# Kernel tuning notes

Hardware: AMD Instinct MI355X
Metric: run time of the kernel (lower is better)

Reference implementation:

```python
import jax, jax.numpy as jnp
import numpy as np

B_, C_, H_, W_ = 4, 96, 256, 256
COUT = 96  # c2


def dwt(x):
    # Haar decompose over 2x2 blocks; names mirror the torch code:
    # x1_1 = even-row/even-col, x2_1 = odd-row/even-col,
    # x1_2 = even-row/odd-col,  x2_2 = odd-row/odd-col (all /2).
    x1_1 = x[:, :, 0::2, 0::2] * 0.5
    x2_1 = x[:, :, 1::2, 0::2] * 0.5
    x1_2 = x[:, :, 0::2, 1::2] * 0.5
    x2_2 = x[:, :, 1::2, 1::2] * 0.5
    A = x1_1 + x2_1 + x1_2 + x2_2
    Bc = -x1_1 - x2_1 + x1_2 + x2_2
    Cc = -x1_1 + x2_1 - x1_2 + x2_2
    D = x1_1 - x2_1 - x1_2 + x2_2
    return A, Bc, Cc, D


def idwt(A, Bc, Cc, D):
    q = 0.25
    x1_1 = (A - Bc - Cc + D) * q
    x2_1 = (A - Bc + Cc - D) * q
    x1_2 = (A + Bc - Cc - D) * q
    x2_2 = (A + Bc + Cc + D) * q
    b, c, h, w = x1_1.shape
    # interleave columns: x1[:, :, :, 0::2]=x1_1, x1[:, :, :, 1::2]=x1_2
    x1 = jnp.stack([x1_1, x1_2], axis=-1).reshape(b, c, h, 2 * w)
    x2 = jnp.stack([x2_1, x2_2], axis=-1).reshape(b, c, h, 2 * w)
    # interleave rows with the *2 scaling from the torch code
    x = jnp.stack([x1 * 2.0, x2 * 2.0], axis=3).reshape(b, c, 2 * h, 2 * w)
    return x


def ffm(a, b):
    # mask*a + (1-mask)*b with binary mask == select
    return jnp.where(jnp.abs(a) >= jnp.abs(b), a, b)


def setup_inputs() -> dict:
    key = jax.random.key(0)
    k1, k2, k3, kw = jax.random.split(key, 4)
    shp = (B_, C_, H_, W_)
    x1 = jax.random.normal(k1, shp, dtype=jnp.float32)
    x2 = jax.random.normal(k2, shp, dtype=jnp.float32)
    x3 = jax.random.normal(k3, shp, dtype=jnp.float32)
    w_out = jax.random.normal(kw, (COUT, 3 * C_), dtype=jnp.float32) / np.sqrt(3 * C_).astype(np.float32)
    return {"x1": x1, "x2": x2, "x3": x3, "w_out": w_out}


def reference(x1, x2, x3, w_out):
    # same channels / same even HxW -> no align conv, no interpolate, no pad
    A1, B1, C1, D1 = dwt(x1)
    A2, B2, C2, D2 = dwt(x2)
    A3, B3, C3, D3 = dwt(x3)
    A = (A1 + A2 + A3) / 3.0
    Bb = ffm(ffm(B1, B2), B3)
    Cc = ffm(ffm(C1, C2), C3)
    Dd = ffm(ffm(D1, D2), D3)
    x_rec = idwt(A, Bb, Cc, Dd)
    y = jnp.concatenate([x_rec, x2, x3], axis=1)  # [B, 3C, H, W]
    return jnp.einsum('bchw,oc->bohw', y, w_out)  # 1x1 conv, no bias
```

## Files before the change

### kernel.cpp

```cpp
#include <hip/hip_runtime.h>

constexpr int NB = 4, NC = 96, NH = 256, NW = 256;
constexpr int NK = 288;
constexpr int HW = NH * NW;

typedef __attribute__((ext_vector_type(8))) short short8;
typedef __attribute__((ext_vector_type(4))) float f32x4;

__device__ __forceinline__ unsigned short f2bf(float f) {
    unsigned int u = __builtin_bit_cast(unsigned int, f);
    u += 0x7FFFu + ((u >> 16) & 1u);
    return (unsigned short)(u >> 16);
}

__device__ __forceinline__ float ffm_sel(float a, float b) {
    return (__builtin_fabsf(a) >= __builtin_fabsf(b)) ? a : b;
}

__global__ __launch_bounds__(256) void dwt_fused_kernel(
    const float* __restrict__ x1, const float* __restrict__ x2,
    const float* __restrict__ x3, const float* __restrict__ w_out,
    float* __restrict__ out)
{
    __shared__ __align__(16) unsigned short y_lds[3][64][40];
    __shared__ __align__(16) unsigned short w_lds[3][96][40];

    const int tid  = threadIdx.x;
    const int wv   = tid >> 6;
    const int lane = tid & 63;
    const int n    = lane & 15;
    const int q    = lane >> 4;
    const int bx = blockIdx.x, by = blockIdx.y, bz = blockIdx.z;

    f32x4 acc[6];
#pragma unroll
    for (int t = 0; t < 6; ++t) acc[t] = (f32x4){0.f, 0.f, 0.f, 0.f};

    const int cp = tid >> 4, cb = tid & 15;
    const int gx = bx * 32 + 2 * cb;
    const int h0 = by * 2;

    for (int s = 0; s < 3; ++s) {
        const int ch0 = 32 * s;

#pragma unroll
        for (int j = 0; j < 9; ++j) {
            int i = tid + (j << 8);
            int row = i >> 3, part = i & 7;
            int sec = (row >= 192) ? 2 : (row >= 96 ? 1 : 0);
            int o = row - sec * 96;
            float4 v = *(const float4*)(w_out + (size_t)o * NK + sec * 96 + ch0 + part * 4);
            *(ushort4*)&w_lds[sec][o][part * 4] =
                make_ushort4(f2bf(v.x), f2bf(v.y), f2bf(v.z), f2bf(v.w));
        }

        float xr[2][4], r2[2][4], r3[2][4];
#pragma unroll
        for (int dc = 0; dc < 2; ++dc) {
            const int c = ch0 + 2 * cp + dc;
            const size_t base = ((size_t)(bz * NC + c) * NH + h0) * NW + gx;
            float2 a1 = *(const float2*)(x1 + base);
            float2 b1 = *(const float2*)(x1 + base + NW);
            float2 a2 = *(const float2*)(x2 + base);
            float2 b2 = *(const float2*)(x2 + base + NW);
            float2 a3 = *(const float2*)(x3 + base);
            float2 b3 = *(const float2*)(x3 + base + NW);

            float A1, B1, C1, D1, A2, B2, C2, D2, A3, B3, C3, D3;
#define DWT4(aa, bb, Ao, Bo, Co, Do)                                          \
            { float e = aa.x * 0.5f, f = bb.x * 0.5f,                          \
                    g = aa.y * 0.5f, h = bb.y * 0.5f;                          \
              Ao = ((e + f) + g) + h;  Bo = (((-e) - f) + g) + h;              \
              Co = (((-e) + f) - g) + h; Do = ((e - f) - g) + h; }
            DWT4(a1, b1, A1, B1, C1, D1)
            DWT4(a2, b2, A2, B2, C2, D2)
            DWT4(a3, b3, A3, B3, C3, D3)
#undef DWT4
            float A  = (A1 + A2 + A3) / 3.0f;
            float Bf = ffm_sel(ffm_sel(B1, B2), B3);
            float Cf = ffm_sel(ffm_sel(C1, C2), C3);
            float Df = ffm_sel(ffm_sel(D1, D2), D3);
            xr[dc][0] = (((A - Bf) - Cf) + Df) * 0.5f;
            xr[dc][1] = (((A - Bf) + Cf) - Df) * 0.5f;
            xr[dc][2] = (((A + Bf) - Cf) - Df) * 0.5f;
            xr[dc][3] = (((A + Bf) + Cf) + Df) * 0.5f;
            r2[dc][0] = a2.x; r2[dc][1] = b2.x; r2[dc][2] = a2.y; r2[dc][3] = b2.y;
            r3[dc][0] = a3.x; r3[dc][1] = b3.x; r3[dc][2] = a3.y; r3[dc][3] = b3.y;
        }
        const int pxs[4] = {2 * cb, 32 + 2 * cb, 2 * cb + 1, 33 + 2 * cb};
#pragma unroll
        for (int p = 0; p < 4; ++p) {
            *(ushort2*)&y_lds[0][pxs[p]][2 * cp] = make_ushort2(f2bf(xr[0][p]), f2bf(xr[1][p]));
            *(ushort2*)&y_lds[1][pxs[p]][2 * cp] = make_ushort2(f2bf(r2[0][p]), f2bf(r2[1][p]));
            *(ushort2*)&y_lds[2][pxs[p]][2 * cp] = make_ushort2(f2bf(r3[0][p]), f2bf(r3[1][p]));
        }

        __syncthreads();

#pragma unroll
        for (int sec = 0; sec < 3; ++sec) {
            short8 bfrag = *(const short8*)&y_lds[sec][16 * wv + n][q * 8];
#pragma unroll
            for (int t = 0; t < 6; ++t) {
                short8 afrag = *(const short8*)&w_lds[sec][16 * t + n][q * 8];
                acc[t] = __builtin_amdgcn_mfma_f32_16x16x32_bf16(afrag, bfrag, acc[t], 0, 0, 0);
            }
        }

        __syncthreads();
    }

    const int row  = wv >> 1;
    const int colb = 16 * (wv & 1) + n;
    const int h    = 2 * by + row;
    const int wc   = 32 * bx + colb;
#pragma unroll
    for (int t = 0; t < 6; ++t) {
#pragma unroll
        for (int r = 0; r < 4; ++r) {
            int o = 16 * t + 4 * q + r;
            out[(size_t)(bz * NC + o) * HW + h * NW + wc] = acc[t][r];
        }
    }
}

extern "C" void kernel_launch(void* const* d_in, const int* in_sizes, int n_in,
                              void* d_out, int out_size, void* d_ws, size_t ws_size,
                              hipStream_t stream) {
    const float* x1 = (const float*)d_in[0];
    const float* x2 = (const float*)d_in[1];
    const float* x3 = (const float*)d_in[2];
    const float* w  = (const float*)d_in[3];
    float* out = (float*)d_out;
    dim3 grid(NW / 32, NH / 2, NB);
    dwt_fused_kernel<<<grid, dim3(256), 0, stream>>>(x1, x2, x3, w, out);
}
```

Measured before the change: 352.5 us.

## Keep weights in registers, loop over row-pairs with double-buffered swizzled LDS

Each block now processes 8 row-pairs with 384 threads instead of one row-pair with 256. The bf16 weight fragments are loaded once into registers per wave (each wave owns 16 output channels), so the per-block LDS weight staging and conversion go away. Global loads for the next row-pair are issued before the current MFMAs, and the staging uses a double-buffered, XOR-swizzled LDS tile that holds all 288 channels at once. The cost is higher register pressure (9 weight fragments plus 36 prefetch floats), a larger LDS footprint, and fewer blocks in the grid.

```diff
diff --git a/kernel.cpp b/kernel.cpp
--- a/kernel.cpp
+++ b/kernel.cpp
@@ -3,6 +3,8 @@
 constexpr int NB = 4, NC = 96, NH = 256, NW = 256;
 constexpr int NK = 288;
 constexpr int HW = NH * NW;
+constexpr int RPB = 8;
+constexpr int ROWB = 640;
 
 typedef __attribute__((ext_vector_type(8))) short short8;
 typedef __attribute__((ext_vector_type(4))) float f32x4;
@@ -17,109 +19,152 @@
     return (__builtin_fabsf(a) >= __builtin_fabsf(b)) ? a : b;
 }
 
-__global__ __launch_bounds__(256) void dwt_fused_kernel(
+__global__ __launch_bounds__(384, 3) void dwt_fused_kernel(
     const float* __restrict__ x1, const float* __restrict__ x2,
     const float* __restrict__ x3, const float* __restrict__ w_out,
     float* __restrict__ out)
 {
-    __shared__ __align__(16) unsigned short y_lds[3][64][40];
-    __shared__ __align__(16) unsigned short w_lds[3][96][40];
+    __shared__ __align__(16) unsigned char y_lds[2][64 * ROWB];
 
     const int tid  = threadIdx.x;
     const int wv   = tid >> 6;
     const int lane = tid & 63;
-    const int n    = lane & 15;
-    const int q    = lane >> 4;
+    const int n = lane & 15;
+    const int q = lane >> 4;
     const int bx = blockIdx.x, by = blockIdx.y, bz = blockIdx.z;
 
-    f32x4 acc[6];
+    short8 wfrag[9];
+    {
+        const float* wr = w_out + (size_t)(16 * wv + n) * NK + 8 * q;
 #pragma unroll
-    for (int t = 0; t < 6; ++t) acc[t] = (f32x4){0.f, 0.f, 0.f, 0.f};
+        for (int c9 = 0; c9 < 9; ++c9) {
+            float4 lo = *(const float4*)(wr + 32 * c9);
+            float4 hi = *(const float4*)(wr + 32 * c9 + 4);
+            short8 f;
+            f[0] = (short)f2bf(lo.x); f[1] = (short)f2bf(lo.y);
+            f[2] = (short)f2bf(lo.z); f[3] = (short)f2bf(lo.w);
+            f[4] = (short)f2bf(hi.x); f[5] = (short)f2bf(hi.y);
+            f[6] = (short)f2bf(hi.z); f[7] = (short)f2bf(hi.w);
+            wfrag[c9] = f;
+        }
+    }
 
-    const int cp = tid >> 4, cb = tid & 15;
-    const int gx = bx * 32 + 2 * cb;
-    const int h0 = by * 2;
+    const int cp = tid >> 3;
+    const int cq = tid & 7;
+    const int gx = bx * 32 + 4 * cq;
+    const float* xs[3] = {x1, x2, x3};
 
-    for (int s = 0; s < 3; ++s) {
-        const int ch0 = 32 * s;
+    float4 pf[3][2][2];
 
+    auto issue = [&](int rp) {
+        const int h0 = 2 * (by * RPB + rp);
 #pragma unroll
-        for (int j = 0; j < 9; ++j) {
-            int i = tid + (j << 8);
-            int row = i >> 3, part = i & 7;
-            int sec = (row >= 192) ? 2 : (row >= 96 ? 1 : 0);
-            int o = row - sec * 96;
-            float4 v = *(const float4*)(w_out + (size_t)o * NK + sec * 96 + ch0 + part * 4);
-            *(ushort4*)&w_lds[sec][o][part * 4] =
-                make_ushort4(f2bf(v.x), f2bf(v.y), f2bf(v.z), f2bf(v.w));
+        for (int a = 0; a < 3; ++a) {
+#pragma unroll
+            for (int dc = 0; dc < 2; ++dc) {
+                const int c = 2 * cp + dc;
+                const size_t base = ((size_t)(bz * NC + c) * NH + h0) * NW + gx;
+                pf[a][dc][0] = *(const float4*)(xs[a] + base);
+                pf[a][dc][1] = *(const float4*)(xs[a] + base + NW);
+            }
         }
+    };
 
-        float xr[2][4], r2[2][4], r3[2][4];
+    auto stage = [&](int buf) {
+        unsigned char* Y = y_lds[buf];
 #pragma unroll
-        for (int dc = 0; dc < 2; ++dc) {
-            const int c = ch0 + 2 * cp + dc;
-            const size_t base = ((size_t)(bz * NC + c) * NH + h0) * NW + gx;
-            float2 a1 = *(const float2*)(x1 + base);
-            float2 b1 = *(const float2*)(x1 + base + NW);
-            float2 a2 = *(const float2*)(x2 + base);
-            float2 b2 = *(const float2*)(x2 + base + NW);
-            float2 a3 = *(const float2*)(x3 + base);
-            float2 b3 = *(const float2*)(x3 + base + NW);
+        for (int hf = 0; hf < 2; ++hf) {
+            const int cb = 2 * cq + hf;
+            float xr[2][4], r2[2][4], r3[2][4];
+#pragma unroll
+            for (int dc = 0; dc < 2; ++dc) {
+                float2 a1, b1, a2, b2, a3, b3;
+                if (hf == 0) {
+                    a1 = make_float2(pf[0][dc][0].x, pf[0][dc][0].y);
+                    b1 = make_float2(pf[0][dc][1].x, pf[0][dc][1].y);
+                    a2 = make_float2(pf[1][dc][0].x, pf[1][dc][0].y);
+                    b2 = make_float2(pf[1][dc][1].x, pf[1][dc][1].y);
+                    a3 = make_float2(pf[2][dc][0].x, pf[2][dc][0].y);
+                    b3 = make_float2(pf[2][dc][1].x, pf[2][dc][1].y);
+                } else {
+                    a1 = make_float2(pf[0][dc][0].z, pf[0][dc][0].w);
+                    b1 = make_float2(pf[0][dc][1].z, pf[0][dc][1].w);
+                    a2 = make_float2(pf[1][dc][0].z, pf[1][dc][0].w);
+                    b2 = make_float2(pf[1][dc][1].z, pf[1][dc][1].w);
+                    a3 = make_float2(pf[2][dc][0].z, pf[2][dc][0].w);
+                    b3 = make_float2(pf[2][dc][1].z, pf[2][dc][1].w);
+                }
+                float A1, B1, C1, D1, A2, B2, C2, D2, A3, B3, C3, D3;
+#define DWT4(aa, bb, Ao, Bo, Co, Do)                                          \
+                { float e = aa.x * 0.5f, fE = bb.x * 0.5f,                     \
+                        g = aa.y * 0.5f, hE = bb.y * 0.5f;                     \
+                  Ao = ((e + fE) + g) + hE;  Bo = (((-e) - fE) + g) + hE;      \
+                  Co = (((-e) + fE) - g) + hE; Do = ((e - fE) - g) + hE; }
+                DWT4(a1, b1, A1, B1, C1, D1)
+                DWT4(a2, b2, A2, B2, C2, D2)
+                DWT4(a3, b3, A3, B3, C3, D3)
+#undef DWT4
+                float A  = (A1 + A2 + A3) / 3.0f;
+                float Bf = ffm_sel(ffm_sel(B1, B2), B3);
+                float Cf = ffm_sel(ffm_sel(C1, C2), C3);
+                float Df = ffm_sel(ffm_sel(D1, D2), D3);
+                xr[dc][0] = (((A - Bf) - Cf) + Df) * 0.5f;
+                xr[dc][1] = (((A - Bf) + Cf) - Df) * 0.5f;
+                xr[dc][2] = (((A + Bf) - Cf) - Df) * 0.5f;
+                xr[dc][3] = (((A + Bf) + Cf) + Df) * 0.5f;
+                r2[dc][0] = a2.x; r2[dc][1] = b2.x; r2[dc][2] = a2.y; r2[dc][3] = b2.y;
+                r3[dc][0] = a3.x; r3[dc][1] = b3.x; r3[dc][2] = a3.y; r3[dc][3] = b3.y;
+            }
+            const int pxs[4] = {2 * cb, 32 + 2 * cb, 2 * cb + 1, 33 + 2 * cb};
+#pragma unroll
+            for (int p = 0; p < 4; ++p) {
+                const int px = pxs[p];
+                unsigned char* rowp = Y + px * ROWB;
+                const int sw = ((px ^ (px >> 3)) & 7) << 4;
+                *(ushort2*)(rowp + ((      4 * cp) ^ sw)) = make_ushort2(f2bf(xr[0][p]), f2bf(xr[1][p]));
+                *(ushort2*)(rowp + ((192 + 4 * cp) ^ sw)) = make_ushort2(f2bf(r2[0][p]), f2bf(r2[1][p]));
+                *(ushort2*)(rowp + ((384 + 4 * cp) ^ sw)) = make_ushort2(f2bf(r3[0][p]), f2bf(r3[1][p]));
+            }
+        }
+    };
 
-            float A1, B1, C1, D1, A2, B2, C2, D2, A3, B3, C3, D3;
-#define DWT4(aa, bb, Ao, Bo, Co, Do)                                          \
-            { float e = aa.x * 0.5f, f = bb.x * 0.5f,                          \
-                    g = aa.y * 0.5f, h = bb.y * 0.5f;                          \
-              Ao = ((e + f) + g) + h;  Bo = (((-e) - f) + g) + h;              \
-              Co = (((-e) + f) - g) + h; Do = ((e - f) - g) + h; }
-            DWT4(a1, b1, A1, B1, C1, D1)
-            DWT4(a2, b2, A2, B2, C2, D2)
-            DWT4(a3, b3, A3, B3, C3, D3)
-#undef DWT4
-            float A  = (A1 + A2 + A3) / 3.0f;
-            float Bf = ffm_sel(ffm_sel(B1, B2), B3);
-            float Cf = ffm_sel(ffm_sel(C1, C2), C3);
-            float Df = ffm_sel(ffm_sel(D1, D2), D3);
-            xr[dc][0] = (((A - Bf) - Cf) + Df) * 0.5f;
-            xr[dc][1] = (((A - Bf) + Cf) - Df) * 0.5f;
-            xr[dc][2] = (((A + Bf) - Cf) - Df) * 0.5f;
-            xr[dc][3] = (((A + Bf) + Cf) + Df) * 0.5f;
-            r2[dc][0] = a2.x; r2[dc][1] = b2.x; r2[dc][2] = a2.y; r2[dc][3] = b2.y;
-            r3[dc][0] = a3.x; r3[dc][1] = b3.x; r3[dc][2] = a3.y; r3[dc][3] = b3.y;
-        }
-        const int pxs[4] = {2 * cb, 32 + 2 * cb, 2 * cb + 1, 33 + 2 * cb};
+    issue(0);
+    stage(0);
+    __syncthreads();
+
+    for (int rp = 0; rp < RPB; ++rp) {
+        const int cur = rp & 1;
+        if (rp + 1 < RPB) issue(rp + 1);
+
+        const unsigned char* Y = y_lds[cur];
+        f32x4 acc[4];
 #pragma unroll
-        for (int p = 0; p < 4; ++p) {
-            *(ushort2*)&y_lds[0][pxs[p]][2 * cp] = make_ushort2(f2bf(xr[0][p]), f2bf(xr[1][p]));
-            *(ushort2*)&y_lds[1][pxs[p]][2 * cp] = make_ushort2(f2bf(r2[0][p]), f2bf(r2[1][p]));
-            *(ushort2*)&y_lds[2][pxs[p]][2 * cp] = make_ushort2(f2bf(r3[0][p]), f2bf(r3[1][p]));
-        }
-
-        __syncthreads();
-
+        for (int pt = 0; pt < 4; ++pt) acc[pt] = (f32x4){0.f, 0.f, 0.f, 0.f};
 #pragma unroll
-        for (int sec = 0; sec < 3; ++sec) {
-            short8 bfrag = *(const short8*)&y_lds[sec][16 * wv + n][q * 8];
+        for (int pt = 0; pt < 4; ++pt) {
+            const int px = 16 * pt + n;
+            const unsigned char* rowp = Y + px * ROWB;
+            const int sw = ((px ^ (px >> 3)) & 7) << 4;
 #pragma unroll
-            for (int t = 0; t < 6; ++t) {
-                short8 afrag = *(const short8*)&w_lds[sec][16 * t + n][q * 8];
-                acc[t] = __builtin_amdgcn_mfma_f32_16x16x32_bf16(afrag, bfrag, acc[t], 0, 0, 0);
+            for (int c9 = 0; c9 < 9; ++c9) {
+                short8 bfrag = *(const short8*)(rowp + ((64 * c9 + 16 * q) ^ sw));
+                acc[pt] = __builtin_amdgcn_mfma_f32_16x16x32_bf16(wfrag[c9], bfrag, acc[pt], 0, 0, 0);
             }
         }
 
-        __syncthreads();
-    }
+        const int h0 = 2 * (by * RPB + rp);
+#pragma unroll
+        for (int pt = 0; pt < 4; ++pt) {
+            const int h  = h0 + (pt >> 1);
+            const int wc = bx * 32 + 16 * (pt & 1) + n;
+            float* op = out + (size_t)(bz * NC + 16 * wv + 4 * q) * HW + (size_t)h * NW + wc;
+#pragma unroll
+            for (int r = 0; r < 4; ++r) op[(size_t)r * HW] = acc[pt][r];
+        }
 
-    const int row  = wv >> 1;
-    const int colb = 16 * (wv & 1) + n;
-    const int h    = 2 * by + row;
-    const int wc   = 32 * bx + colb;
-#pragma unroll
-    for (int t = 0; t < 6; ++t) {
-#pragma unroll
-        for (int r = 0; r < 4; ++r) {
-            int o = 16 * t + 4 * q + r;
-            out[(size_t)(bz * NC + o) * HW + h * NW + wc] = acc[t][r];
+        if (rp + 1 < RPB) {
+            stage(cur ^ 1);
+            __syncthreads();
         }
     }
 }
@@ -132,6 +177,6 @@
     const float* x3 = (const float*)d_in[2];
     const float* w  = (const float*)d_in[3];
     float* out = (float*)d_out;
-    dim3 grid(NW / 32, NH / 2, NB);
-    dwt_fused_kernel<<<grid, dim3(256), 0, stream>>>(x1, x2, x3, w, out);
+    dim3 grid(NW / 32, NH / (2 * RPB), NB);
+    dwt_fused_kernel<<<grid, dim3(384), 0, stream>>>(x1, x2, x3, w, out);
 }
```

Result: slower. 496.5 us (+40.8%).
